# Performance work log

Hardware: AMD Instinct MI355X
Metric: run time of the kernel (lower is better)

Reference implementation:

```python
import math
import jax, jax.numpy as jnp
import numpy as np

B, S, T = 32, 512, 180
D, F, L, H = 512, 2048, 6, 8
DH = D // H


def _pos_encoding(length, d):
    pos = np.arange(length, dtype=np.float32)[:, None]
    div = np.exp(np.arange(0, d, 2, dtype=np.float32) * (-math.log(10000.0) / d))
    pe = np.zeros((length, d), dtype=np.float32)
    pe[:, 0::2] = np.sin(pos * div)
    pe[:, 1::2] = np.cos(pos * div)
    return jnp.asarray(pe)


def _ln(x, scale, bias):
    mu = x.mean(-1, keepdims=True)
    var = ((x - mu) ** 2).mean(-1, keepdims=True)
    return (x - mu) * jax.lax.rsqrt(var + 1e-5) * scale + bias


def _mha(q_in, kv_in, w, b, causal=False):
    # w: [4, D, D] = (Wq, Wk, Wv, Wo); b: [4, D]
    b_, sq = q_in.shape[:2]
    q = (q_in @ w[0] + b[0]).reshape(b_, sq, H, DH)
    k = (kv_in @ w[1] + b[1]).reshape(b_, -1, H, DH)
    v = (kv_in @ w[2] + b[2]).reshape(b_, -1, H, DH)
    s = jnp.einsum('bqhd,bkhd->bhqk', q, k) / math.sqrt(DH)
    if causal:
        mask = jnp.tril(jnp.ones((sq, k.shape[1]), dtype=bool))
        s = jnp.where(mask, s, -1e9)
    a = jax.nn.softmax(s, axis=-1)
    o = jnp.einsum('bhqk,bkhd->bqhd', a, v).reshape(b_, sq, D)
    return o @ w[3] + b[3]


def _ffn(x, w1, b1, w2, b2):
    return jax.nn.relu(x @ w1 + b1) @ w2 + b2


def setup_inputs() -> dict:
    key = jax.random.key(0)
    ks = jax.random.split(key, 16)
    n = lambda k, shape: jax.random.normal(k, shape, jnp.float32) * 0.02
    return {
        'x': jax.random.normal(ks[0], (B, S, 2), jnp.float32),
        'y_cv_teacher': jax.random.normal(ks[1], (B, T, 1), jnp.float32),
        'src_proj_w': n(ks[2], (2, D)), 'src_proj_b': jnp.zeros((D,), jnp.float32),
        'tgt_proj_w': n(ks[3], (1, D)), 'tgt_proj_b': jnp.zeros((D,), jnp.float32),
        'enc_attn_w': n(ks[4], (L, 4, D, D)), 'enc_attn_b': jnp.zeros((L, 4, D), jnp.float32),
        'enc_ffn_w1': n(ks[5], (L, D, F)), 'enc_ffn_b1': jnp.zeros((L, F), jnp.float32),
        'enc_ffn_w2': n(ks[6], (L, F, D)), 'enc_ffn_b2': jnp.zeros((L, D), jnp.float32),
        'enc_ln_scale': jnp.ones((L, 2, D), jnp.float32), 'enc_ln_bias': jnp.zeros((L, 2, D), jnp.float32),
        'dec_self_w': n(ks[7], (L, 4, D, D)), 'dec_self_b': jnp.zeros((L, 4, D), jnp.float32),
        'dec_cross_w': n(ks[8], (L, 4, D, D)), 'dec_cross_b': jnp.zeros((L, 4, D), jnp.float32),
        'dec_ffn_w1': n(ks[9], (L, D, F)), 'dec_ffn_b1': jnp.zeros((L, F), jnp.float32),
        'dec_ffn_w2': n(ks[10], (L, F, D)), 'dec_ffn_b2': jnp.zeros((L, D), jnp.float32),
        'dec_ln_scale': jnp.ones((L, 3, D), jnp.float32), 'dec_ln_bias': jnp.zeros((L, 3, D), jnp.float32),
        'out_w': n(ks[11], (D, 1)), 'out_b': jnp.zeros((1,), jnp.float32),
    }


def reference(x, y_cv_teacher, src_proj_w, src_proj_b, tgt_proj_w, tgt_proj_b,
              enc_attn_w, enc_attn_b, enc_ffn_w1, enc_ffn_b1, enc_ffn_w2, enc_ffn_b2,
              enc_ln_scale, enc_ln_bias, dec_self_w, dec_self_b, dec_cross_w, dec_cross_b,
              dec_ffn_w1, dec_ffn_b1, dec_ffn_w2, dec_ffn_b2, dec_ln_scale, dec_ln_bias,
              out_w, out_b):
    pe = _pos_encoding(512, D)
    # encoder (post-norm, relu FFN, dropout disabled = eval semantics)
    h = x @ src_proj_w + src_proj_b + pe[: x.shape[1]]
    for i in range(L):
        h = _ln(h + _mha(h, h, enc_attn_w[i], enc_attn_b[i]), enc_ln_scale[i, 0], enc_ln_bias[i, 0])
        h = _ln(h + _ffn(h, enc_ffn_w1[i], enc_ffn_b1[i], enc_ffn_w2[i], enc_ffn_b2[i]),
                enc_ln_scale[i, 1], enc_ln_bias[i, 1])
    memory = h
    # teacher-forced decoder input: [start=0, y_cv_teacher[:-1]]
    tgt_in = jnp.concatenate([jnp.zeros((x.shape[0], 1, 1), x.dtype), y_cv_teacher[:, :-1, :]], axis=1)
    d = tgt_in @ tgt_proj_w + tgt_proj_b + pe[: tgt_in.shape[1]]
    for i in range(L):
        d = _ln(d + _mha(d, d, dec_self_w[i], dec_self_b[i], causal=True),
                dec_ln_scale[i, 0], dec_ln_bias[i, 0])
        d = _ln(d + _mha(d, memory, dec_cross_w[i], dec_cross_b[i]),
                dec_ln_scale[i, 1], dec_ln_bias[i, 1])
        d = _ln(d + _ffn(d, dec_ffn_w1[i], dec_ffn_b1[i], dec_ffn_w2[i], dec_ffn_b2[i]),
                dec_ln_scale[i, 2], dec_ln_bias[i, 2])
    return d @ out_w + out_b  # [B, T, 1]
```

## Files before the change

### kernel.cpp

```cpp
#include <hip/hip_runtime.h>
#include <math.h>

#define B_  32
#define S_  512
#define T_  180
#define D_  512
#define F_  2048
#define L_  6
#define H_  8
#define DH_ 64

typedef unsigned short u16;
typedef __attribute__((ext_vector_type(8))) short short8;
typedef __attribute__((ext_vector_type(4))) float floatx4;

__device__ __forceinline__ float bf2f(u16 h) {
    union { unsigned u; float f; } un; un.u = ((unsigned)h) << 16; return un.f;
}
__device__ __forceinline__ u16 f2bf(float f) {
    union { float f; unsigned u; } un; un.f = f;
    unsigned u = un.u;
    u += 0x7fffu + ((u >> 16) & 1u);
    return (u16)(u >> 16);
}

__device__ __forceinline__ void gload16(const u16* g, u16* l) {
    __builtin_amdgcn_global_load_lds(
        (const __attribute__((address_space(1))) void*)g,
        (__attribute__((address_space(3))) void*)l, 16, 0, 0);
}

__device__ __forceinline__ float pos_enc(int pos, int c) {
    int i2 = c & ~1;
    float div = expf(-(float)i2 * (9.210340371976184f / 512.0f));
    float arg = (float)pos * div;
    return (c & 1) ? cosf(arg) : sinf(arg);
}

__global__ __launch_bounds__(256) void embed_src_kernel(
    const float* __restrict__ x, const float* __restrict__ w,
    const float* __restrict__ b, u16* __restrict__ h)
{
    int idx = blockIdx.x * 256 + threadIdx.x;
    if (idx >= B_ * S_ * D_) return;
    int c  = idx & (D_ - 1);
    int bs = idx >> 9;
    int s  = bs & (S_ - 1);
    float x0 = x[bs * 2 + 0];
    float x1 = x[bs * 2 + 1];
    h[idx] = f2bf(x0 * w[c] + x1 * w[D_ + c] + b[c] + pos_enc(s, c));
}

__global__ __launch_bounds__(256) void embed_tgt_kernel(
    const float* __restrict__ y, const float* __restrict__ w,
    const float* __restrict__ b, u16* __restrict__ d)
{
    int idx = blockIdx.x * 256 + threadIdx.x;
    if (idx >= B_ * T_ * D_) return;
    int c  = idx & (D_ - 1);
    int bt = idx >> 9;
    int t  = bt % T_;
    int bb = bt / T_;
    float tv = (t == 0) ? 0.0f : y[bb * T_ + (t - 1)];
    d[idx] = f2bf(tv * w[c] + b[c] + pos_enc(t, c));
}

__global__ __launch_bounds__(256) void wconv_kernel(
    const float* __restrict__ W, u16* __restrict__ Wt, int K, int N)
{
    __shared__ float tile[32][33];
    size_t mat = (size_t)blockIdx.z * K * N;
    const float* Wm = W + mat;
    u16* Wtm = Wt + mat;
    int n0 = blockIdx.x * 32, k0 = blockIdx.y * 32;
    int tx = threadIdx.x & 31, ty = threadIdx.x >> 5;
#pragma unroll
    for (int i = 0; i < 32; i += 8)
        tile[ty + i][tx] = Wm[(size_t)(k0 + ty + i) * N + n0 + tx];
    __syncthreads();
#pragma unroll
    for (int i = 0; i < 32; i += 8)
        Wtm[(size_t)(n0 + ty + i) * K + k0 + tx] = f2bf(tile[tx][ty + i]);
}

__global__ __launch_bounds__(256) void gemm_bf16_kernel(
    const u16* __restrict__ A, int lda, const u16* __restrict__ Bt,
    const float* __restrict__ bias, u16* __restrict__ C, int ldc,
    int M, int N, int K, int relu)
{
    __shared__ u16 smem[18432];
    u16* As = smem;
    u16* Bs = smem + 4096;

    int tid  = threadIdx.x;
    int w    = tid >> 6;
    int lane = tid & 63;
    int m0 = blockIdx.y << 7, n0 = blockIdx.x << 7;

    int sr = w * 32 + (lane >> 2);
    int sk = (lane & 3) * 8;
    const u16* ag0 = A  + (size_t)(m0 + sr)      * lda + sk;
    const u16* ag1 = A  + (size_t)(m0 + sr + 16) * lda + sk;
    const u16* bg0 = Bt + (size_t)(n0 + sr)      * K + sk;
    const u16* bg1 = Bt + (size_t)(n0 + sr + 16) * K + sk;
    u16* al0 = As + (w * 2 + 0) * 512;
    u16* al1 = As + (w * 2 + 1) * 512;
    u16* bl0 = Bs + (w * 2 + 0) * 512;
    u16* bl1 = Bs + (w * 2 + 1) * 512;

    int wm = (w >> 1) * 64, wn = (w & 1) * 64;
    int fr = lane & 15;
    int fk = (lane >> 4) * 8;

    floatx4 acc[4][4] = {};

    for (int k0 = 0; k0 < K; k0 += 32) {
        gload16(ag0 + k0, al0);
        gload16(ag1 + k0, al1);
        gload16(bg0 + k0, bl0);
        gload16(bg1 + k0, bl1);
        __syncthreads();

        short8 af[4], bf[4];
#pragma unroll
        for (int i = 0; i < 4; ++i)
            af[i] = *(const short8*)&As[(wm + i * 16 + fr) * 32 + fk];
#pragma unroll
        for (int j = 0; j < 4; ++j)
            bf[j] = *(const short8*)&Bs[(wn + j * 16 + fr) * 32 + fk];
#pragma unroll
        for (int i = 0; i < 4; ++i)
#pragma unroll
            for (int j = 0; j < 4; ++j)
                acc[i][j] = __builtin_amdgcn_mfma_f32_16x16x32_bf16(
                    af[i], bf[j], acc[i][j], 0, 0, 0);
        __syncthreads();
    }

    u16* epi = smem + w * 4608;
    int cc = lane & 15;
    int rq = (lane >> 4) * 4;
#pragma unroll
    for (int j = 0; j < 4; ++j) {
        float bj = bias[n0 + wn + j * 16 + cc];
#pragma unroll
        for (int i = 0; i < 4; ++i) {
#pragma unroll
            for (int r = 0; r < 4; ++r) {
                float vv = acc[i][j][r] + bj;
                if (relu) vv = fmaxf(vv, 0.f);
                epi[(i * 16 + rq + r) * 72 + j * 16 + cc] = f2bf(vv);
            }
        }
    }
    __syncthreads();
#pragma unroll
    for (int t = 0; t < 8; ++t) {
        int er = t * 8 + (lane >> 3);
        int ec = (lane & 7) * 8;
        short8 vv = *(const short8*)&epi[er * 72 + ec];
        *(short8*)&C[(size_t)(m0 + wm + er) * ldc + n0 + wn + ec] = vv;
    }
}

__global__ __launch_bounds__(256) void attn_mfma_kernel(
    const u16* Q, int qs, const u16* __restrict__ K, int ks,
    const u16* __restrict__ V, u16* O,
    int Sq, int Sk, int causal)
{
    __shared__ u16 Qs[64 * 72];
    __shared__ u16 Ks[64 * 72];
    __shared__ u16 Vt[64 * 72];
    __shared__ u16 Ps[4][16 * 72];

    int tid  = threadIdx.x;
    int w    = tid >> 6;
    int lane = tid & 63;
    int n    = lane & 15;
    int quad = lane >> 4;
    int q0 = blockIdx.x * 64;
    int hh = blockIdx.y, bb = blockIdx.z;

    const u16* Qb = Q + (size_t)bb * Sq * qs + hh * DH_;
    const u16* Kb = K + (size_t)bb * Sk * ks + hh * DH_;
    const u16* Vb = V + (size_t)bb * Sk * ks + hh * DH_;

#pragma unroll
    for (int it = 0; it < 2; ++it) {
        int idx = it * 256 + tid;
        int r = idx >> 3, dg = (idx & 7) * 8;
        int qg = q0 + r;
        short8 vv = {};
        if (qg < Sq) vv = *(const short8*)&Qb[(size_t)qg * qs + dg];
        *(short8*)&Qs[r * 72 + dg] = vv;
    }

    float m_i[4], l_i[4];
    floatx4 o_acc[4] = {};
#pragma unroll
    for (int r = 0; r < 4; ++r) { m_i[r] = -1e30f; l_i[r] = 0.f; }

    int qrow0 = q0 + w * 16 + quad * 4;
    int kend = causal ? ((Sk < q0 + 64) ? Sk : (q0 + 64)) : Sk;
    __syncthreads();

    for (int k0 = 0; k0 < kend; k0 += 64) {
#pragma unroll
        for (int it = 0; it < 2; ++it) {
            int idx = it * 256 + tid;
            int r = idx >> 3, dg = (idx & 7) * 8;
            int kg = k0 + r;
            short8 kv = {}, vv = {};
            if (kg < Sk) {
                kv = *(const short8*)&Kb[(size_t)kg * ks + dg];
                vv = *(const short8*)&Vb[(size_t)kg * ks + dg];
            }
            *(short8*)&Ks[r * 72 + dg] = kv;
            int col = (r + dg) & 63;
#pragma unroll
            for (int j = 0; j < 8; ++j)
                Vt[(dg + j) * 72 + col] = (u16)vv[j];
        }
        __syncthreads();

        floatx4 sc[4] = {};
        short8 aq0 = *(const short8*)&Qs[(w * 16 + n) * 72 + quad * 8];
        short8 aq1 = *(const short8*)&Qs[(w * 16 + n) * 72 + 32 + quad * 8];
#pragma unroll
        for (int j = 0; j < 4; ++j) {
            short8 bk0 = *(const short8*)&Ks[(j * 16 + n) * 72 + quad * 8];
            short8 bk1 = *(const short8*)&Ks[(j * 16 + n) * 72 + 32 + quad * 8];
            sc[j] = __builtin_amdgcn_mfma_f32_16x16x32_bf16(aq0, bk0, sc[j], 0, 0, 0);
            sc[j] = __builtin_amdgcn_mfma_f32_16x16x32_bf16(aq1, bk1, sc[j], 0, 0, 0);
        }

#pragma unroll
        for (int j = 0; j < 4; ++j) {
            int kg = k0 + j * 16 + n;
#pragma unroll
            for (int r = 0; r < 4; ++r) {
                float s = sc[j][r] * 0.125f;
                if (kg >= Sk || (causal && kg > qrow0 + r)) s = -1e9f;
                sc[j][r] = s;
            }
        }

#pragma unroll
        for (int r = 0; r < 4; ++r) {
            float mx = fmaxf(fmaxf(sc[0][r], sc[1][r]), fmaxf(sc[2][r], sc[3][r]));
#pragma unroll
            for (int off = 8; off > 0; off >>= 1)
                mx = fmaxf(mx, __shfl_xor(mx, off, 16));
            float mnew = fmaxf(m_i[r], mx);
            float alpha = __expf(m_i[r] - mnew);
            m_i[r] = mnew;
            float ps = 0.f;
#pragma unroll
            for (int j = 0; j < 4; ++j) {
                float p = __expf(sc[j][r] - mnew);
                sc[j][r] = p; ps += p;
            }
#pragma unroll
            for (int off = 8; off > 0; off >>= 1)
                ps += __shfl_xor(ps, off, 16);
            l_i[r] = l_i[r] * alpha + ps;
#pragma unroll
            for (int jb = 0; jb < 4; ++jb) o_acc[jb][r] *= alpha;
        }

#pragma unroll
        for (int j = 0; j < 4; ++j)
#pragma unroll
            for (int r = 0; r < 4; ++r)
                Ps[w][(quad * 4 + r) * 72 + j * 16 + n] = f2bf(sc[j][r]);

        short8 ap0 = *(const short8*)&Ps[w][n * 72 + quad * 8];
        short8 ap1 = *(const short8*)&Ps[w][n * 72 + 32 + quad * 8];
#pragma unroll
        for (int jb = 0; jb < 4; ++jb) {
            int d = jb * 16 + n;
            int rot = d & ~7;
            short8 bv0 = *(const short8*)&Vt[d * 72 + ((quad * 8 + rot) & 63)];
            short8 bv1 = *(const short8*)&Vt[d * 72 + ((32 + quad * 8 + rot) & 63)];
            o_acc[jb] = __builtin_amdgcn_mfma_f32_16x16x32_bf16(ap0, bv0, o_acc[jb], 0, 0, 0);
            o_acc[jb] = __builtin_amdgcn_mfma_f32_16x16x32_bf16(ap1, bv1, o_acc[jb], 0, 0, 0);
        }
        __syncthreads();
    }

    float inv[4];
#pragma unroll
    for (int r = 0; r < 4; ++r) inv[r] = 1.0f / l_i[r];
    u16* Ob = O + (size_t)bb * Sq * qs + hh * DH_;
#pragma unroll
    for (int r = 0; r < 4; ++r) {
        int qg = qrow0 + r;
        if (qg < Sq) {
#pragma unroll
            for (int jb = 0; jb < 4; ++jb)
                Ob[(size_t)qg * qs + jb * 16 + n] = f2bf(o_acc[jb][r] * inv[r]);
        }
    }
}

__global__ __launch_bounds__(128) void add_ln_kernel(
    u16* __restrict__ h, const u16* __restrict__ delta,
    const float* __restrict__ scale, const float* __restrict__ bias)
{
    __shared__ float red[2][2];
    int row = blockIdx.x, tid = threadIdx.x;
    int lane = tid & 63, wv = tid >> 6;
    size_t base = (size_t)row * D_ + tid * 4;
    uint2 hv = *(const uint2*)&h[base];
    uint2 dv = *(const uint2*)&delta[base];
    float v0 = bf2f(hv.x & 0xffff) + bf2f(dv.x & 0xffff);
    float v1 = bf2f(hv.x >> 16)    + bf2f(dv.x >> 16);
    float v2 = bf2f(hv.y & 0xffff) + bf2f(dv.y & 0xffff);
    float v3 = bf2f(hv.y >> 16)    + bf2f(dv.y >> 16);

    float a  = v0 + v1 + v2 + v3;
    float b2 = v0 * v0 + v1 * v1 + v2 * v2 + v3 * v3;
#pragma unroll
    for (int off = 32; off > 0; off >>= 1) {
        a  += __shfl_xor(a, off);
        b2 += __shfl_xor(b2, off);
    }
    if (lane == 0) { red[wv][0] = a; red[wv][1] = b2; }
    __syncthreads();
    float S1 = red[0][0] + red[1][0];
    float S2 = red[0][1] + red[1][1];
    float mu = S1 * (1.0f / 512.0f);
    float var = S2 * (1.0f / 512.0f) - mu * mu;
    float rs = rsqrtf(var + 1e-5f);

    int c = tid * 4;
    float4 sc = *(const float4*)&scale[c];
    float4 bi = *(const float4*)&bias[c];
    unsigned lo = (unsigned)f2bf((v0 - mu) * rs * sc.x + bi.x) |
                  ((unsigned)f2bf((v1 - mu) * rs * sc.y + bi.y) << 16);
    unsigned hi = (unsigned)f2bf((v2 - mu) * rs * sc.z + bi.z) |
                  ((unsigned)f2bf((v3 - mu) * rs * sc.w + bi.w) << 16);
    *(uint2*)&h[base] = make_uint2(lo, hi);
}

__global__ __launch_bounds__(64) void out_proj_kernel(
    const u16* __restrict__ d, const float* __restrict__ w,
    const float* __restrict__ b, float* __restrict__ out)
{
    int row = blockIdx.x, lane = threadIdx.x;
    float s = 0.f;
    for (int c = lane; c < D_; c += 64) s += bf2f(d[(size_t)row * D_ + c]) * w[c];
#pragma unroll
    for (int off = 32; off > 0; off >>= 1) s += __shfl_down(s, off);
    if (lane == 0) out[row] = s + b[0];
}

extern "C" void kernel_launch(void* const* d_in, const int* in_sizes, int n_in,
                              void* d_out, int out_size, void* d_ws, size_t ws_size,
                              hipStream_t stream)
{
    const float* x          = (const float*)d_in[0];
    const float* y          = (const float*)d_in[1];
    const float* src_w      = (const float*)d_in[2];
    const float* src_b      = (const float*)d_in[3];
    const float* tgt_w      = (const float*)d_in[4];
    const float* tgt_b      = (const float*)d_in[5];
    const float* enc_attn_w = (const float*)d_in[6];
    const float* enc_attn_b = (const float*)d_in[7];
    const float* enc_ffn_w1 = (const float*)d_in[8];
    const float* enc_ffn_b1 = (const float*)d_in[9];
    const float* enc_ffn_w2 = (const float*)d_in[10];
    const float* enc_ffn_b2 = (const float*)d_in[11];
    const float* enc_ln_s   = (const float*)d_in[12];
    const float* enc_ln_b   = (const float*)d_in[13];
    const float* dec_self_w = (const float*)d_in[14];
    const float* dec_self_b = (const float*)d_in[15];
    const float* dec_cross_w= (const float*)d_in[16];
    const float* dec_cross_b= (const float*)d_in[17];
    const float* dec_ffn_w1 = (const float*)d_in[18];
    const float* dec_ffn_b1 = (const float*)d_in[19];
    const float* dec_ffn_w2 = (const float*)d_in[20];
    const float* dec_ffn_b2 = (const float*)d_in[21];
    const float* dec_ln_s   = (const float*)d_in[22];
    const float* dec_ln_b   = (const float*)d_in[23];
    const float* out_w      = (const float*)d_in[24];
    const float* out_b      = (const float*)d_in[25];
    float* out = (float*)d_out;

    const size_t E_BSD = (size_t)B_ * S_ * D_;
    const size_t E_BTD = (size_t)B_ * T_ * D_;
    const size_t WDD   = (size_t)D_ * D_;
    const size_t WDF   = (size_t)D_ * F_;
    const int MS = B_ * S_;
    const int MT = B_ * T_;

    u16* h    = (u16*)d_ws;
    u16* qkv  = h + E_BSD;
    u16* o    = qkv + (size_t)MS * 1536;
    u16* dbuf = o + E_BSD;
    u16* wsc  = dbuf + E_BTD;
    u16* mid  = qkv;
    u16* cq   = qkv;
    u16* ckv  = qkv + 4 * 1024 * 1024;

    auto gemm = [&](const u16* A, int lda, const u16* Wt, const float* bi,
                    u16* C, int ldc, int M, int N, int K, int relu) {
        dim3 g(N / 128, M / 128);
        gemm_bf16_kernel<<<g, dim3(256), 0, stream>>>(A, lda, Wt, bi, C, ldc,
                                                      M, N, K, relu);
    };
    auto attn = [&](const u16* Qp, int qs, const u16* Kp, int ks,
                    const u16* Vp, u16* Op, int Sq, int Sk, int causal) {
        dim3 g((Sq + 63) / 64, H_, B_);
        attn_mfma_kernel<<<g, dim3(256), 0, stream>>>(Qp, qs, Kp, ks, Vp, Op,
                                                      Sq, Sk, causal);
    };
    auto addln = [&](u16* hp, const u16* dp, const float* sc, const float* bi,
                     int rows) {
        add_ln_kernel<<<dim3(rows), dim3(128), 0, stream>>>(hp, dp, sc, bi);
    };
    auto wconv = [&](const float* W, u16* Wt, int K, int N, int nmat) {
        wconv_kernel<<<dim3(N / 32, K / 32, nmat), dim3(256), 0, stream>>>(W, Wt, K, N);
    };

    embed_src_kernel<<<dim3((B_ * S_ * D_ + 255) / 256), dim3(256), 0, stream>>>(
        x, src_w, src_b, h);
    for (int l = 0; l < L_; ++l) {
        wconv(enc_attn_w + (size_t)l * 4 * WDD, wsc, D_, D_, 4);
        wconv(enc_ffn_w1 + (size_t)l * WDF, wsc + 4 * WDD, D_, F_, 1);
        wconv(enc_ffn_w2 + (size_t)l * WDF, wsc + 4 * WDD + WDF, F_, D_, 1);

        const float* bl = enc_attn_b + (size_t)l * 4 * D_;
        gemm(h, D_, wsc, bl, qkv, 1536, MS, 1536, D_, 0);
        attn(qkv, 1536, qkv + 512, 1536, qkv + 1024, qkv, S_, S_, 0);
        gemm(qkv, 1536, wsc + 3 * WDD, bl + 3 * D_, o, D_, MS, D_, D_, 0);
        addln(h, o, enc_ln_s + (size_t)l * 2 * D_, enc_ln_b + (size_t)l * 2 * D_, MS);

        for (int m0 = 0; m0 < MS; m0 += 8192) {
            gemm(h + (size_t)m0 * D_, D_, wsc + 4 * WDD,
                 enc_ffn_b1 + (size_t)l * F_, mid, F_, 8192, F_, D_, 1);
            gemm(mid, F_, wsc + 4 * WDD + WDF, enc_ffn_b2 + (size_t)l * D_,
                 o + (size_t)m0 * D_, D_, 8192, D_, F_, 0);
        }
        addln(h, o, enc_ln_s + (size_t)l * 2 * D_ + D_,
              enc_ln_b + (size_t)l * 2 * D_ + D_, MS);
    }

    embed_tgt_kernel<<<dim3((B_ * T_ * D_ + 255) / 256), dim3(256), 0, stream>>>(
        y, tgt_w, tgt_b, dbuf);
    for (int l = 0; l < L_; ++l) {
        wconv(dec_self_w  + (size_t)l * 4 * WDD, wsc, D_, D_, 4);
        wconv(dec_cross_w + (size_t)l * 4 * WDD, wsc + 4 * WDD, D_, D_, 4);
        wconv(dec_ffn_w1  + (size_t)l * WDF, wsc + 8 * WDD, D_, F_, 1);
        wconv(dec_ffn_w2  + (size_t)l * WDF, wsc + 8 * WDD + WDF, F_, D_, 1);

        const float* bl = dec_self_b + (size_t)l * 4 * D_;
        gemm(dbuf, D_, wsc, bl, qkv, 1536, MT, 1536, D_, 0);
        attn(qkv, 1536, qkv + 512, 1536, qkv + 1024, qkv, T_, T_, 1);
        gemm(qkv, 1536, wsc + 3 * WDD, bl + 3 * D_, o, D_, MT, D_, D_, 0);
        addln(dbuf, o, dec_ln_s + (size_t)l * 3 * D_,
              dec_ln_b + (size_t)l * 3 * D_, MT);

        const float* bc = dec_cross_b + (size_t)l * 4 * D_;
        gemm(h, D_, wsc + 5 * WDD, bc + D_, ckv, 1024, MS, 1024, D_, 0);
        gemm(dbuf, D_, wsc + 4 * WDD, bc, cq, D_, MT, D_, D_, 0);
        attn(cq, 512, ckv, 1024, ckv + 512, cq, T_, S_, 0);
        gemm(cq, D_, wsc + 7 * WDD, bc + 3 * D_, o, D_, MT, D_, D_, 0);
        addln(dbuf, o, dec_ln_s + (size_t)l * 3 * D_ + D_,
              dec_ln_b + (size_t)l * 3 * D_ + D_, MT);

        gemm(dbuf, D_, wsc + 8 * WDD, dec_ffn_b1 + (size_t)l * F_,
             mid, F_, MT, F_, D_, 1);
        gemm(mid, F_, wsc + 8 * WDD + WDF, dec_ffn_b2 + (size_t)l * D_,
             o, D_, MT, D_, F_, 0);
        addln(dbuf, o, dec_ln_s + (size_t)l * 3 * D_ + 2 * D_,
              dec_ln_b + (size_t)l * 3 * D_ + 2 * D_, MT);
    }

    out_proj_kernel<<<dim3(MT), dim3(64), 0, stream>>>(dbuf, out_w, out_b, out);
}
```

Baseline: 3.769 ms.

## Double GEMM K-step to 64 and streamline attention softmax, masking, grid order

Result: faster. 3.495 ms (-7.3%).

```diff
diff --git a/kernel.cpp b/kernel.cpp
--- a/kernel.cpp
+++ b/kernel.cpp
@@ -90,7 +90,7 @@
 {
     __shared__ u16 smem[18432];
     u16* As = smem;
-    u16* Bs = smem + 4096;
+    u16* Bs = smem + 8192;
 
     int tid  = threadIdx.x;
     int w    = tid >> 6;
@@ -114,26 +114,35 @@
 
     floatx4 acc[4][4] = {};
 
-    for (int k0 = 0; k0 < K; k0 += 32) {
-        gload16(ag0 + k0, al0);
-        gload16(ag1 + k0, al1);
-        gload16(bg0 + k0, bl0);
-        gload16(bg1 + k0, bl1);
+    for (int k0 = 0; k0 < K; k0 += 64) {
+#pragma unroll
+        for (int hh = 0; hh < 2; ++hh) {
+            int go = k0 + hh * 32;
+            int lo = hh * 4096;
+            gload16(ag0 + go, al0 + lo);
+            gload16(ag1 + go, al1 + lo);
+            gload16(bg0 + go, bl0 + lo);
+            gload16(bg1 + go, bl1 + lo);
+        }
         __syncthreads();
 
-        short8 af[4], bf[4];
-#pragma unroll
-        for (int i = 0; i < 4; ++i)
-            af[i] = *(const short8*)&As[(wm + i * 16 + fr) * 32 + fk];
-#pragma unroll
-        for (int j = 0; j < 4; ++j)
-            bf[j] = *(const short8*)&Bs[(wn + j * 16 + fr) * 32 + fk];
-#pragma unroll
-        for (int i = 0; i < 4; ++i)
+#pragma unroll
+        for (int hh = 0; hh < 2; ++hh) {
+            int lo = hh * 4096;
+            short8 af[4], bf[4];
+#pragma unroll
+            for (int i = 0; i < 4; ++i)
+                af[i] = *(const short8*)&As[lo + (wm + i * 16 + fr) * 32 + fk];
 #pragma unroll
             for (int j = 0; j < 4; ++j)
-                acc[i][j] = __builtin_amdgcn_mfma_f32_16x16x32_bf16(
-                    af[i], bf[j], acc[i][j], 0, 0, 0);
+                bf[j] = *(const short8*)&Bs[lo + (wn + j * 16 + fr) * 32 + fk];
+#pragma unroll
+            for (int i = 0; i < 4; ++i)
+#pragma unroll
+                for (int j = 0; j < 4; ++j)
+                    acc[i][j] = __builtin_amdgcn_mfma_f32_16x16x32_bf16(
+                        af[i], bf[j], acc[i][j], 0, 0, 0);
+        }
         __syncthreads();
     }
 
@@ -163,6 +172,8 @@
     }
 }
 
+#define CEXP 0.1803368801111244f
+
 __global__ __launch_bounds__(256) void attn_mfma_kernel(
     const u16* Q, int qs, const u16* __restrict__ K, int ks,
     const u16* __restrict__ V, u16* O,
@@ -178,12 +189,13 @@
     int lane = tid & 63;
     int n    = lane & 15;
     int quad = lane >> 4;
-    int q0 = blockIdx.x * 64;
-    int hh = blockIdx.y, bb = blockIdx.z;
-
-    const u16* Qb = Q + (size_t)bb * Sq * qs + hh * DH_;
-    const u16* Kb = K + (size_t)bb * Sk * ks + hh * DH_;
-    const u16* Vb = V + (size_t)bb * Sk * ks + hh * DH_;
+    int bh = blockIdx.x;
+    int bb = bh >> 3, hhd = bh & 7;
+    int q0 = blockIdx.y * 64;
+
+    const u16* Qb = Q + (size_t)bb * Sq * qs + hhd * DH_;
+    const u16* Kb = K + (size_t)bb * Sk * ks + hhd * DH_;
+    const u16* Vb = V + (size_t)bb * Sk * ks + hhd * DH_;
 
 #pragma unroll
     for (int it = 0; it < 2; ++it) {
@@ -234,14 +246,17 @@
             sc[j] = __builtin_amdgcn_mfma_f32_16x16x32_bf16(aq1, bk1, sc[j], 0, 0, 0);
         }
 
-#pragma unroll
-        for (int j = 0; j < 4; ++j) {
-            int kg = k0 + j * 16 + n;
-#pragma unroll
-            for (int r = 0; r < 4; ++r) {
-                float s = sc[j][r] * 0.125f;
-                if (kg >= Sk || (causal && kg > qrow0 + r)) s = -1e9f;
-                sc[j][r] = s;
+        bool need_mask = (k0 + 64 > Sk) ||
+                         (causal && (k0 + 63 > q0 + w * 16));
+        if (need_mask) {
+#pragma unroll
+            for (int j = 0; j < 4; ++j) {
+                int kg = k0 + j * 16 + n;
+#pragma unroll
+                for (int r = 0; r < 4; ++r) {
+                    if (kg >= Sk || (causal && kg > qrow0 + r))
+                        sc[j][r] = -1e30f;
+                }
             }
         }
 
@@ -252,12 +267,12 @@
             for (int off = 8; off > 0; off >>= 1)
                 mx = fmaxf(mx, __shfl_xor(mx, off, 16));
             float mnew = fmaxf(m_i[r], mx);
-            float alpha = __expf(m_i[r] - mnew);
+            float alpha = exp2f((m_i[r] - mnew) * CEXP);
             m_i[r] = mnew;
             float ps = 0.f;
 #pragma unroll
             for (int j = 0; j < 4; ++j) {
-                float p = __expf(sc[j][r] - mnew);
+                float p = exp2f((sc[j][r] - mnew) * CEXP);
                 sc[j][r] = p; ps += p;
             }
 #pragma unroll
@@ -291,7 +306,7 @@
     float inv[4];
 #pragma unroll
     for (int r = 0; r < 4; ++r) inv[r] = 1.0f / l_i[r];
-    u16* Ob = O + (size_t)bb * Sq * qs + hh * DH_;
+    u16* Ob = O + (size_t)bb * Sq * qs + hhd * DH_;
 #pragma unroll
     for (int r = 0; r < 4; ++r) {
         int qg = qrow0 + r;
@@ -411,7 +426,7 @@
     };
     auto attn = [&](const u16* Qp, int qs, const u16* Kp, int ks,
                     const u16* Vp, u16* Op, int Sq, int Sk, int causal) {
-        dim3 g((Sq + 63) / 64, H_, B_);
+        dim3 g(B_ * H_, (Sq + 63) / 64);
         attn_mfma_kernel<<<g, dim3(256), 0, stream>>>(Qp, qs, Kp, ks, Vp, Op,
                                                       Sq, Sk, causal);
     };
```
